# Kernel optimization log

Hardware: AMD Instinct MI355X
Metric: run time of the kernel (lower is better)

Reference implementation:

```python
import jax, jax.numpy as jnp
import numpy as np

B, L, D = 16, 2048, 128


def setup_inputs() -> dict:
    key = jax.random.key(0)
    k1, k2 = jax.random.split(key)
    x = jax.random.normal(k1, (B, L, D), dtype=jnp.float32)
    mask = jax.random.uniform(k2, (B, L), dtype=jnp.float32)
    return {"input": x, "mask": mask}


def reference(input, mask):
    # mask broadcast over feature dim (torch: mask.unsqueeze(-1).repeat(1,1,D))
    x = input * mask[:, :, None]                       # [B, L, D]
    # attn_weights = bmm(x, x^T) -> [B, L, L]
    scores = jnp.einsum('bld,bmd->blm', x, x)
    # softmax over dim=1 (the FIRST L axis, i.e. columns normalized over rows)
    w = jax.nn.softmax(scores, axis=1)                 # [B, L, L]
    # out = bmm(w^T, x).mean(dim=1, keepdim=True): out_full[b,m,d] = sum_l w[b,l,m] * x[b,l,d]
    out = jnp.einsum('blm,bld->bmd', w, x).mean(axis=1, keepdims=True)  # [B, 1, D]
    attn_mean = w.mean(axis=1)                         # [B, L]
    return (out, attn_mean)
```

## Files before the change

### kernel.cpp

```cpp
#include <hip/hip_runtime.h>
#include <math.h>


constexpr int NB = 16, NL = 2048, ND = 128;
constexpr int ROWS_US = 128;
constexpr int NSLOT = 24;

typedef __attribute__((ext_vector_type(8))) short short8;
typedef __attribute__((ext_vector_type(4))) float f32x4;

#define EXP2(x) __builtin_amdgcn_exp2f(x)

__device__ __forceinline__ unsigned short f2bf(float f) {
  unsigned u = __builtin_bit_cast(unsigned, f);
  u += 0x7FFFu + ((u >> 16) & 1u);
  return (unsigned short)(u >> 16);
}
__device__ __forceinline__ float bf2f(unsigned short h) {
  unsigned u = ((unsigned)h) << 16;
  return __builtin_bit_cast(float, u);
}

__device__ __forceinline__ void stage16(const unsigned short* g, unsigned short* l) {
  __builtin_amdgcn_global_load_lds(
      (const __attribute__((address_space(1))) unsigned int*)g,
      (__attribute__((address_space(3))) unsigned int*)l, 16, 0, 0);
}

__global__ __launch_bounds__(256) void k_prep(const float* __restrict__ x,
                                              const float* __restrict__ mask,
                                              unsigned short* __restrict__ Y,
                                              float* __restrict__ nsq,
                                              float* __restrict__ am) {
  const int gid = blockIdx.x * 256 + threadIdx.x;
  if (gid < NB * NL) am[gid] = 1.0f / NL;
  const int row = gid >> 5;
  const int dq = gid & 31;
  const float4 v = reinterpret_cast<const float4*>(x)[gid];
  const float m = mask[row] * 1.2011224087864498f;
  const unsigned short h0 = f2bf(v.x * m), h1 = f2bf(v.y * m),
                       h2 = f2bf(v.z * m), h3 = f2bf(v.w * m);
  const float g0 = bf2f(h0), g1 = bf2f(h1), g2 = bf2f(h2), g3 = bf2f(h3);
  unsigned short* Yr = Y + (size_t)row * ROWS_US;
  const int sx = dq >> 1, half8 = (dq & 1) * 4;
  const int pos = sx ^ (row & 15);
  *reinterpret_cast<ushort4*>(Yr + pos * 8 + half8) = make_ushort4(h0, h1, h2, h3);
  float ss = g0 * g0 + g1 * g1 + g2 * g2 + g3 * g3;
#pragma unroll
  for (int mk = 1; mk < 32; mk <<= 1) ss += __shfl_xor(ss, mk);
  if (dq == 0) nsq[row] = ss;
}

__global__ __launch_bounds__(256) void k_nmax(const float* __restrict__ nsq,
                                              float* __restrict__ nmax) {
  const int b = blockIdx.x;
  const int tid = threadIdx.x;
  float m = 0.f;
  for (int i = tid; i < NL; i += 256) m = fmaxf(m, nsq[b * NL + i]);
#pragma unroll
  for (int mk = 1; mk < 64; mk <<= 1) m = fmaxf(m, __shfl_xor(m, mk));
  __shared__ float red[4];
  if ((tid & 63) == 0) red[tid >> 6] = m;
  __syncthreads();
  if (tid == 0) nmax[b] = fmaxf(fmaxf(red[0], red[1]), fmaxf(red[2], red[3]));
}

#define STRIP_DECODE()                                     \
  const int sid = blockIdx.x;                              \
  const int idx = sid >> 3;                                \
  const int b = ((sid & 7) << 1) | (idx >> 5);             \
  const int strip = idx & 31;                              \
  const int ib = strip >> 1, hf = strip & 1;               \
  const int d0 = hf * 4;                                   \
  const int nt = (hf == 0) ? 4 : ((ib < 8) ? 5 : 4);       \
  const int row0 = ib * 128;                               \
  const int tid = threadIdx.x;                             \
  const int lane = tid & 63, wave = tid >> 6;              \
  const int wr = wave >> 2, wc = wave & 3;                 \
  const int lhi = lane >> 4, llo = lane & 15;

#define STAGE_T(dst, Yb, r0)                                                \
  _Pragma("unroll") for (int it = 0; it < 4; ++it) {                        \
    const int idx2 = tid + 512 * it;                                        \
    const int r = idx2 >> 4, s = idx2 & 15;                                 \
    stage16((Yb) + (size_t)((r0) + r) * ROWS_US + s * 8, (dst) + idx2 * 8); \
  }

#define TILE_MFMA(Atp, Btp)                                                  \
  f32x4 acc[4][2];                                                           \
  _Pragma("unroll") for (int rs = 0; rs < 4; ++rs)                           \
      _Pragma("unroll") for (int cs = 0; cs < 2; ++cs)                       \
          acc[rs][cs] = f32x4{0.f, 0.f, 0.f, 0.f};                           \
  _Pragma("unroll") for (int t4 = 0; t4 < 4; ++t4) {                         \
    const int sl = 4 * t4 + lhi;                                             \
    short8 af[4], bf[2];                                                     \
    _Pragma("unroll") for (int qq = 0; qq < 4; ++qq) {                       \
      const int ra = 64 * wr + 16 * qq + llo;                                \
      af[qq] = *(const short8*)((Atp) + ra * 128 + ((sl ^ (ra & 15)) << 3)); \
    }                                                                        \
    _Pragma("unroll") for (int cs = 0; cs < 2; ++cs) {                       \
      const int rb = 32 * wc + 16 * cs + llo;                                \
      bf[cs] = *(const short8*)((Btp) + rb * 128 + ((sl ^ (rb & 15)) << 3)); \
    }                                                                        \
    _Pragma("unroll") for (int rs = 0; rs < 4; ++rs)                         \
        _Pragma("unroll") for (int cs = 0; cs < 2; ++cs)                     \
            acc[rs][cs] = __builtin_amdgcn_mfma_f32_16x16x32_bf16(           \
                af[rs], bf[cs], acc[rs][cs], 0, 0, 0);                       \
  }

__global__ __launch_bounds__(512, 4) void k_esum(const unsigned short* __restrict__ Y,
                                                 const float* __restrict__ nsq,
                                                 const float* __restrict__ nmaxf,
                                                 float* __restrict__ pcs) {
  __shared__ alignas(128) char lds[65536];
  unsigned short* At = (unsigned short*)lds;
  unsigned short* Bt = (unsigned short*)(lds + 32768);
  STRIP_DECODE()
  const unsigned short* Yb = Y + (size_t)b * NL * ROWS_US;
  const float Nmx = nmaxf[b];

  float Cr[16];
#pragma unroll
  for (int rs = 0; rs < 4; ++rs)
#pragma unroll
    for (int rg = 0; rg < 4; ++rg)
      Cr[rs * 4 + rg] = sqrtf(nsq[b * NL + row0 + 64 * wr + 16 * rs + 4 * lhi + rg] * Nmx);

  STAGE_T(At, Yb, row0)

  float racc[16];
#pragma unroll
  for (int i = 0; i < 16; ++i) racc[i] = 0.f;

  for (int dt = 0; dt < nt; ++dt) {
    const int d = d0 + dt;
    const int col0 = ((ib + d) & 15) * 128;
    __syncthreads();
    STAGE_T(Bt, Yb, col0)
    float Cc[2];
#pragma unroll
    for (int cs = 0; cs < 2; ++cs)
      Cc[cs] = sqrtf(nsq[b * NL + col0 + 32 * wc + 16 * cs + llo] * Nmx);
    __syncthreads();
    TILE_MFMA(At, Bt)
#pragma unroll
    for (int rs = 0; rs < 4; ++rs)
#pragma unroll
      for (int rg = 0; rg < 4; ++rg)
        racc[rs * 4 + rg] += EXP2(acc[rs][0][rg] - Cr[rs * 4 + rg]) +
                             EXP2(acc[rs][1][rg] - Cr[rs * 4 + rg]);
    if (d != 0) {
      float* dst = pcs + ((size_t)(b * NSLOT + 8 + 2 * (d - 1) + wr)) * NL + col0;
#pragma unroll
      for (int cs = 0; cs < 2; ++cs) {
        float u = 0.f;
#pragma unroll
        for (int rs = 0; rs < 4; ++rs)
#pragma unroll
          for (int rg = 0; rg < 4; ++rg) u += EXP2(acc[rs][cs][rg] - Cc[cs]);
        u += __shfl_xor(u, 16);
        u += __shfl_xor(u, 32);
        if (lhi == 0) dst[32 * wc + 16 * cs + llo] = u;
      }
    }
  }
#pragma unroll
  for (int i = 0; i < 16; ++i) {
    float s = racc[i];
#pragma unroll
    for (int mk = 1; mk < 16; mk <<= 1) s += __shfl_xor(s, mk);
    racc[i] = s;
  }
  if (llo == 0) {
    float* dst = pcs + ((size_t)(b * NSLOT + 4 * hf + wc)) * NL + row0;
#pragma unroll
    for (int rs = 0; rs < 4; ++rs)
#pragma unroll
      for (int rg = 0; rg < 4; ++rg)
        dst[64 * wr + 16 * rs + 4 * lhi + rg] = racc[rs * 4 + rg];
  }
}

__global__ __launch_bounds__(256) void k_comb(const float* __restrict__ pcs,
                                              const float* __restrict__ nsq,
                                              const float* __restrict__ nmaxf,
                                              float* __restrict__ Q) {
  const int i = blockIdx.x * 256 + threadIdx.x;
  const int b = i >> 11, row = i & (NL - 1);
  const int o = row >> 7;
  float s = 0.f;
#pragma unroll
  for (int c = 0; c < NSLOT; ++c) {
    if (c >= 22 && o < 8) continue;
    s += pcs[((size_t)(b * NSLOT + c)) * NL + row];
  }
  Q[i] = -sqrtf(nsq[i] * nmaxf[b]) - __log2f(s);
}

__global__ __launch_bounds__(512, 4) void k_r(const unsigned short* __restrict__ Y,
                                              const float* __restrict__ Qa,
                                              float* __restrict__ rp) {
  __shared__ alignas(128) char lds[65536];
  unsigned short* At = (unsigned short*)lds;
  unsigned short* Bt = (unsigned short*)(lds + 32768);
  STRIP_DECODE()
  const unsigned short* Yb = Y + (size_t)b * NL * ROWS_US;

  float Qr[16];
#pragma unroll
  for (int rs = 0; rs < 4; ++rs)
#pragma unroll
    for (int rg = 0; rg < 4; ++rg)
      Qr[rs * 4 + rg] = Qa[b * NL + row0 + 64 * wr + 16 * rs + 4 * lhi + rg];

  STAGE_T(At, Yb, row0)

  float racc[16];
#pragma unroll
  for (int i = 0; i < 16; ++i) racc[i] = 0.f;

  for (int dt = 0; dt < nt; ++dt) {
    const int d = d0 + dt;
    const int col0 = ((ib + d) & 15) * 128;
    __syncthreads();
    STAGE_T(Bt, Yb, col0)
    float Qc[2];
#pragma unroll
    for (int cs = 0; cs < 2; ++cs)
      Qc[cs] = Qa[b * NL + col0 + 32 * wc + 16 * cs + llo];
    __syncthreads();
    TILE_MFMA(At, Bt)
#pragma unroll
    for (int rs = 0; rs < 4; ++rs)
#pragma unroll
      for (int rg = 0; rg < 4; ++rg)
        racc[rs * 4 + rg] += EXP2(acc[rs][0][rg] + Qc[0]) +
                             EXP2(acc[rs][1][rg] + Qc[1]);
    if (d != 0) {
      float* dst = rp + ((size_t)(b * NSLOT + 8 + 2 * (d - 1) + wr)) * NL + col0;
#pragma unroll
      for (int cs = 0; cs < 2; ++cs) {
        float u = 0.f;
#pragma unroll
        for (int rs = 0; rs < 4; ++rs)
#pragma unroll
          for (int rg = 0; rg < 4; ++rg) u += EXP2(acc[rs][cs][rg] + Qr[rs * 4 + rg]);
        u += __shfl_xor(u, 16);
        u += __shfl_xor(u, 32);
        if (lhi == 0) dst[32 * wc + 16 * cs + llo] = u;
      }
    }
  }
#pragma unroll
  for (int i = 0; i < 16; ++i) {
    float s = racc[i];
#pragma unroll
    for (int mk = 1; mk < 16; mk <<= 1) s += __shfl_xor(s, mk);
    racc[i] = s;
  }
  if (llo == 0) {
    float* dst = rp + ((size_t)(b * NSLOT + 4 * hf + wc)) * NL + row0;
#pragma unroll
    for (int rs = 0; rs < 4; ++rs)
#pragma unroll
      for (int rg = 0; rg < 4; ++rg)
        dst[64 * wr + 16 * rs + 4 * lhi + rg] = racc[rs * 4 + rg];
  }
}

__global__ __launch_bounds__(256) void k_outp(const float* __restrict__ x,
                                              const float* __restrict__ mask,
                                              const float* __restrict__ rp,
                                              float* __restrict__ partial) {
  const int b = blockIdx.y;
  const int seg = blockIdx.x;
  const int tid = threadIdx.x;
  const int l0 = seg * 128;
  __shared__ float w_s[128];
  __shared__ float4 red[8][32];
  if (tid < 128) {
    float s = 0.f;
#pragma unroll
    for (int c = 0; c < NSLOT; ++c) {
      if (c >= 22 && seg < 8) continue;
      s += rp[((size_t)(b * NSLOT + c)) * NL + l0 + tid];
    }
    w_s[tid] = s * mask[b * NL + l0 + tid];
  }
  __syncthreads();
  const int dq = tid & 31;
  const int rg = tid >> 5;
  float4 acc = make_float4(0.f, 0.f, 0.f, 0.f);
#pragma unroll 4
  for (int i = 0; i < 16; ++i) {
    const int l = 8 * i + rg;
    const float w = w_s[l];
    const float4 v = *reinterpret_cast<const float4*>(x + ((size_t)b * NL + l0 + l) * ND + 4 * dq);
    acc.x += w * v.x; acc.y += w * v.y; acc.z += w * v.z; acc.w += w * v.w;
  }
  red[rg][dq] = acc;
  __syncthreads();
  if (rg == 0) {
    float4 s = acc;
#pragma unroll
    for (int k = 1; k < 8; ++k) {
      const float4 t = red[k][dq];
      s.x += t.x; s.y += t.y; s.z += t.z; s.w += t.w;
    }
    *reinterpret_cast<float4*>(partial + ((size_t)(b * 16 + seg)) * ND + 4 * dq) = s;
  }
}

__global__ __launch_bounds__(1024) void k_fin(const float* __restrict__ partial,
                                              float* __restrict__ out) {
  const int gid = blockIdx.x * 1024 + threadIdx.x;
  const int b = gid >> 7, d = gid & (ND - 1);
  float s = 0.f;
#pragma unroll
  for (int k = 0; k < 16; ++k) s += partial[(size_t)(b * 16 + k) * ND + d];
  out[gid] = s * (1.0f / NL);
}

extern "C" void kernel_launch(void* const* d_in, const int* in_sizes, int n_in,
                              void* d_out, int out_size, void* d_ws, size_t ws_size,
                              hipStream_t stream) {
  const float* x = (const float*)d_in[0];
  const float* mask = (const float*)d_in[1];
  float* out = (float*)d_out;

  unsigned short* Y = (unsigned short*)d_ws;
  float* nsq = (float*)(Y + (size_t)NB * NL * ROWS_US);
  float* nmaxf = nsq + NB * NL;
  float* pcs = nmaxf + 16;
  float* rp = pcs;
  float* Q = pcs + (size_t)NB * NSLOT * NL;
  float* partial = Q + NB * NL;

  k_prep<<<dim3(NB * NL * ND / 4 / 256), 256, 0, stream>>>(x, mask, Y, nsq,
                                                           out + NB * ND);
  k_nmax<<<NB, 256, 0, stream>>>(nsq, nmaxf);
  k_esum<<<dim3(512), 512, 0, stream>>>(Y, nsq, nmaxf, pcs);
  k_comb<<<dim3(NB * NL / 256), 256, 0, stream>>>(pcs, nsq, nmaxf, Q);
  k_r<<<dim3(512), 512, 0, stream>>>(Y, Q, rp);
  k_outp<<<dim3(16, NB), 256, 0, stream>>>(x, mask, rp, partial);
  k_fin<<<2, 1024, 0, stream>>>(partial, out);
}
```

Baseline: 66.08 us.

## Fuse row-max and column-combine kernels into the esum and r kernels

Drops the separate k_nmax and k_comb launches. Each k_esum block now recomputes the per-batch max squared norm redundantly, overlapping that with the first tile stage. k_r computes the Q values for its row and column tiles on the fly from the partial sums, and rp now gets its own workspace region because it can no longer alias pcs. This removes two launches and a Q round trip through global memory, at the cost of redundant reductions, extra pcs reads per tile and an extra barrier in each k_r loop iteration.

```diff
diff --git a/kernel.cpp b/kernel.cpp
--- a/kernel.cpp
+++ b/kernel.cpp
@@ -49,20 +49,6 @@
 #pragma unroll
   for (int mk = 1; mk < 32; mk <<= 1) ss += __shfl_xor(ss, mk);
   if (dq == 0) nsq[row] = ss;
-}
-
-__global__ __launch_bounds__(256) void k_nmax(const float* __restrict__ nsq,
-                                              float* __restrict__ nmax) {
-  const int b = blockIdx.x;
-  const int tid = threadIdx.x;
-  float m = 0.f;
-  for (int i = tid; i < NL; i += 256) m = fmaxf(m, nsq[b * NL + i]);
-#pragma unroll
-  for (int mk = 1; mk < 64; mk <<= 1) m = fmaxf(m, __shfl_xor(m, mk));
-  __shared__ float red[4];
-  if ((tid & 63) == 0) red[tid >> 6] = m;
-  __syncthreads();
-  if (tid == 0) nmax[b] = fmaxf(fmaxf(red[0], red[1]), fmaxf(red[2], red[3]));
 }
 
 #define STRIP_DECODE()                                     \
@@ -110,14 +96,27 @@
 
 __global__ __launch_bounds__(512, 4) void k_esum(const unsigned short* __restrict__ Y,
                                                  const float* __restrict__ nsq,
-                                                 const float* __restrict__ nmaxf,
+                                                 float* __restrict__ nmaxf,
                                                  float* __restrict__ pcs) {
-  __shared__ alignas(128) char lds[65536];
+  __shared__ alignas(128) char lds[65600];
   unsigned short* At = (unsigned short*)lds;
   unsigned short* Bt = (unsigned short*)(lds + 32768);
+  float* red8 = (float*)(lds + 65536);
   STRIP_DECODE()
   const unsigned short* Yb = Y + (size_t)b * NL * ROWS_US;
-  const float Nmx = nmaxf[b];
+
+  STAGE_T(At, Yb, row0)
+
+  float mx_ = 0.f;
+  for (int i = tid; i < NL; i += 512) mx_ = fmaxf(mx_, nsq[b * NL + i]);
+#pragma unroll
+  for (int mk = 1; mk < 64; mk <<= 1) mx_ = fmaxf(mx_, __shfl_xor(mx_, mk));
+  if (lane == 0) red8[wave] = mx_;
+  __syncthreads();
+  float Nmx = red8[0];
+#pragma unroll
+  for (int k = 1; k < 8; ++k) Nmx = fmaxf(Nmx, red8[k]);
+  if (tid == 0) nmaxf[b] = Nmx;
 
   float Cr[16];
 #pragma unroll
@@ -125,8 +124,6 @@
 #pragma unroll
     for (int rg = 0; rg < 4; ++rg)
       Cr[rs * 4 + rg] = sqrtf(nsq[b * NL + row0 + 64 * wr + 16 * rs + 4 * lhi + rg] * Nmx);
-
-  STAGE_T(At, Yb, row0)
 
   float racc[16];
 #pragma unroll
@@ -181,39 +178,40 @@
   }
 }
 
-__global__ __launch_bounds__(256) void k_comb(const float* __restrict__ pcs,
+__global__ __launch_bounds__(512, 4) void k_r(const unsigned short* __restrict__ Y,
                                               const float* __restrict__ nsq,
                                               const float* __restrict__ nmaxf,
-                                              float* __restrict__ Q) {
-  const int i = blockIdx.x * 256 + threadIdx.x;
-  const int b = i >> 11, row = i & (NL - 1);
-  const int o = row >> 7;
-  float s = 0.f;
-#pragma unroll
-  for (int c = 0; c < NSLOT; ++c) {
-    if (c >= 22 && o < 8) continue;
-    s += pcs[((size_t)(b * NSLOT + c)) * NL + row];
-  }
-  Q[i] = -sqrtf(nsq[i] * nmaxf[b]) - __log2f(s);
-}
-
-__global__ __launch_bounds__(512, 4) void k_r(const unsigned short* __restrict__ Y,
-                                              const float* __restrict__ Qa,
+                                              const float* __restrict__ pcs,
                                               float* __restrict__ rp) {
-  __shared__ alignas(128) char lds[65536];
+  __shared__ alignas(128) char lds[66560];
   unsigned short* At = (unsigned short*)lds;
   unsigned short* Bt = (unsigned short*)(lds + 32768);
+  float* Qr_s = (float*)(lds + 65536);
+  float* Qc_s = (float*)(lds + 66048);
   STRIP_DECODE()
   const unsigned short* Yb = Y + (size_t)b * NL * ROWS_US;
+  const float Nmx = nmaxf[b];
+
+  STAGE_T(At, Yb, row0)
+
+  if (tid < 128) {
+    const int row = row0 + tid;
+    float s = 0.f;
+#pragma unroll
+    for (int c = 0; c < NSLOT; ++c) {
+      if (c >= 22 && ib < 8) continue;
+      s += pcs[((size_t)(b * NSLOT + c)) * NL + row];
+    }
+    Qr_s[tid] = -sqrtf(nsq[b * NL + row] * Nmx) - __log2f(s);
+  }
+  __syncthreads();
 
   float Qr[16];
 #pragma unroll
   for (int rs = 0; rs < 4; ++rs)
 #pragma unroll
     for (int rg = 0; rg < 4; ++rg)
-      Qr[rs * 4 + rg] = Qa[b * NL + row0 + 64 * wr + 16 * rs + 4 * lhi + rg];
-
-  STAGE_T(At, Yb, row0)
+      Qr[rs * 4 + rg] = Qr_s[64 * wr + 16 * rs + 4 * lhi + rg];
 
   float racc[16];
 #pragma unroll
@@ -221,14 +219,24 @@
 
   for (int dt = 0; dt < nt; ++dt) {
     const int d = d0 + dt;
-    const int col0 = ((ib + d) & 15) * 128;
+    const int jb = (ib + d) & 15;
+    const int col0 = jb * 128;
     __syncthreads();
     STAGE_T(Bt, Yb, col0)
+    if (tid < 128) {
+      const int col = col0 + tid;
+      float s = 0.f;
+#pragma unroll
+      for (int c = 0; c < NSLOT; ++c) {
+        if (c >= 22 && jb < 8) continue;
+        s += pcs[((size_t)(b * NSLOT + c)) * NL + col];
+      }
+      Qc_s[tid] = -sqrtf(nsq[b * NL + col] * Nmx) - __log2f(s);
+    }
+    __syncthreads();
     float Qc[2];
 #pragma unroll
-    for (int cs = 0; cs < 2; ++cs)
-      Qc[cs] = Qa[b * NL + col0 + 32 * wc + 16 * cs + llo];
-    __syncthreads();
+    for (int cs = 0; cs < 2; ++cs) Qc[cs] = Qc_s[32 * wc + 16 * cs + llo];
     TILE_MFMA(At, Bt)
 #pragma unroll
     for (int rs = 0; rs < 4; ++rs)
@@ -332,16 +340,13 @@
   float* nsq = (float*)(Y + (size_t)NB * NL * ROWS_US);
   float* nmaxf = nsq + NB * NL;
   float* pcs = nmaxf + 16;
-  float* rp = pcs;
-  float* Q = pcs + (size_t)NB * NSLOT * NL;
-  float* partial = Q + NB * NL;
+  float* rp = pcs + (size_t)NB * NSLOT * NL;
+  float* partial = rp + (size_t)NB * NSLOT * NL;
 
   k_prep<<<dim3(NB * NL * ND / 4 / 256), 256, 0, stream>>>(x, mask, Y, nsq,
                                                            out + NB * ND);
-  k_nmax<<<NB, 256, 0, stream>>>(nsq, nmaxf);
   k_esum<<<dim3(512), 512, 0, stream>>>(Y, nsq, nmaxf, pcs);
-  k_comb<<<dim3(NB * NL / 256), 256, 0, stream>>>(pcs, nsq, nmaxf, Q);
-  k_r<<<dim3(512), 512, 0, stream>>>(Y, Q, rp);
+  k_r<<<dim3(512), 512, 0, stream>>>(Y, nsq, nmaxf, pcs, rp);
   k_outp<<<dim3(16, NB), 256, 0, stream>>>(x, mask, rp, partial);
   k_fin<<<2, 1024, 0, stream>>>(partial, out);
 }
```

Result: slower. 87.02 us (+31.7%).
